# Kernel optimization log

Hardware: AMD Instinct MI355X
Metric: run time of the kernel (lower is better)

## Reference

```python
import jax, jax.numpy as jnp
import numpy as np

D_QUERY = 512
D_AUDIO = 512
D_OUT = 512
B, HW, S = 16, 4096, 1024


def setup_inputs() -> dict:
    key = jax.random.key(0)
    ks = jax.random.split(key, 8)
    sc_q = 1.0 / np.sqrt(D_QUERY)
    sc_a = 1.0 / np.sqrt(D_AUDIO)
    return {
        "x": jax.random.normal(ks[0], (B, HW, D_QUERY), dtype=jnp.float32),
        "audio_embed": jax.random.normal(ks[1], (B, S, D_AUDIO), dtype=jnp.float32),
        "Wq": jax.random.uniform(ks[2], (D_QUERY, D_OUT), jnp.float32, -sc_q, sc_q),
        "bq": jax.random.uniform(ks[3], (D_OUT,), jnp.float32, -sc_q, sc_q),
        "Wk": jax.random.uniform(ks[4], (D_AUDIO, D_OUT), jnp.float32, -sc_a, sc_a),
        "bk": jax.random.uniform(ks[5], (D_OUT,), jnp.float32, -sc_a, sc_a),
        "Wv": jax.random.uniform(ks[6], (D_AUDIO, D_OUT), jnp.float32, -sc_a, sc_a),
        "bv": jax.random.uniform(ks[7], (D_OUT,), jnp.float32, -sc_a, sc_a),
    }


def reference(x, audio_embed, Wq, bq, Wk, bk, Wv, bv):
    # Linear projections (nn.Linear: y = x @ W^T + b; we store W already transposed)
    Q = x @ Wq + bq                      # [B, HW, D_OUT]
    K = audio_embed @ Wk + bk            # [B, S, D_OUT]
    V = audio_embed @ Wv + bv            # [B, S, D_OUT]
    scale = 1.0 / (K.shape[-1] ** 0.5)   # divide by sqrt(d_out), per source
    scores = jnp.einsum("bnd,bsd->bns", Q, K) * scale  # [B, HW, S]
    attn = jax.nn.softmax(scores, axis=-1)
    return jnp.einsum("bns,bsd->bnd", attn, V)         # [B, HW, D_OUT]
```

## Files before the change

kernel.cpp:

```cpp
#include <hip/hip_runtime.h>
#include <hip/hip_bf16.h>

typedef __attribute__((ext_vector_type(8))) short bf16x8;
typedef __attribute__((ext_vector_type(4))) float f32x4;
typedef __attribute__((ext_vector_type(4))) unsigned short ushort4v;

#define AS1 __attribute__((address_space(1)))
#define AS3 __attribute__((address_space(3)))

__device__ __forceinline__ float bf_bits_to_f(short s) {
  unsigned int u = ((unsigned int)(unsigned short)s) << 16;
  union { unsigned int u; float f; } c; c.u = u; return c.f;
}
__device__ __forceinline__ unsigned short f_to_bf_bits(float f) {
  union { float f; unsigned int u; } c; c.f = f;
  unsigned int r = c.u + 0x7FFFu + ((c.u >> 16) & 1u);
  return (unsigned short)(r >> 16);
}

__device__ __forceinline__ int fsw(int row) { return ((row >> 1) & 3) << 4; }

__global__ __launch_bounds__(256) void cvt_bf16_kernel(const float* __restrict__ in,
                                                       unsigned short* __restrict__ out,
                                                       long n) {
  const long nchunks = n >> 2;
  const long stride = (long)gridDim.x * 256;
  for (long c = (long)blockIdx.x * 256 + threadIdx.x; c < nchunks; c += stride) {
    f32x4 v = *(const f32x4*)(in + c * 4);
    ushort4v o;
    o[0] = f_to_bf_bits(v[0]); o[1] = f_to_bf_bits(v[1]);
    o[2] = f_to_bf_bits(v[2]); o[3] = f_to_bf_bits(v[3]);
    *(ushort4v*)(out + c * 4) = o;
  }
}

__global__ __launch_bounds__(256) void transpose_w_kernel(
    const float* __restrict__ W0, const float* __restrict__ W1, const float* __restrict__ W2,
    unsigned short* __restrict__ T0, unsigned short* __restrict__ T1, unsigned short* __restrict__ T2) {
  const float* W = (blockIdx.z == 0) ? W0 : (blockIdx.z == 1) ? W1 : W2;
  unsigned short* T = (blockIdx.z == 0) ? T0 : (blockIdx.z == 1) ? T1 : T2;
  __shared__ float t[32][33];
  const int tx = threadIdx.x & 31, ty = threadIdx.x >> 5;
  const int n0 = blockIdx.x * 32, k0 = blockIdx.y * 32;
#pragma unroll
  for (int j = 0; j < 4; ++j)
    t[ty + 8 * j][tx] = W[(long)(k0 + ty + 8 * j) * 512 + n0 + tx];
  __syncthreads();
#pragma unroll
  for (int j = 0; j < 4; ++j)
    T[(long)(n0 + ty + 8 * j) * 512 + k0 + tx] = f_to_bf_bits(t[tx][ty + 8 * j]);
}

template <bool BIAS, bool TRANSOUT, bool AFP32>
__global__ __launch_bounds__(256) void gemm_kernel(
    const void* __restrict__ Aptr,
    const unsigned short* __restrict__ BT,
    const float* __restrict__ bias,
    unsigned short* __restrict__ Cout,
    const int K, const float scale,
    const long strideA, const long strideBT, const long strideC, const int ldc,
    const int nx, const int ny) {
  __shared__ unsigned short lds[8192];
  const int nwg = gridDim.x;
  const int chunk = nwg >> 3;
  const int bid = blockIdx.x;
  const int swz = (bid & 7) * chunk + (bid >> 3);
  const int bx = swz % nx;
  const int t1 = swz / nx;
  const int by = t1 % ny;
  const int bz = t1 / ny;

  const int tid = threadIdx.x;
  const int lane = tid & 63;
  const int wv = tid >> 6;
  const int wr = wv >> 1, wc = wv & 1;
  const unsigned short* Ab = (const unsigned short*)Aptr + (long)bz * strideA + (long)by * 128 * K;
  const float* Af = (const float*)Aptr + (long)bz * strideA + (long)by * 128 * K;
  const unsigned short* Bb = BT + (long)bz * strideBT + (long)bx * 128 * K;

  f32x4 acc[4][4];
#pragma unroll
  for (int m = 0; m < 4; ++m)
#pragma unroll
    for (int n = 0; n < 4; ++n) acc[m][n] = (f32x4){0.f, 0.f, 0.f, 0.f};

  const int r15 = lane & 15, g = lane >> 4;
  const int kiters = K >> 5;
  const int asw = fsw(r15);

  int arow[2], acs[2];
#pragma unroll
  for (int i = 0; i < 2; ++i) {
    const int c = i * 4 + wv;
    const int boff = c * 1024 + lane * 16;
    arow[i] = boff >> 6;
    acs[i] = (boff & 63) ^ fsw(arow[i]);
  }
  f32x4 pa[2][2];
  if (AFP32) {
#pragma unroll
    for (int i = 0; i < 2; ++i) {
      const float* s = Af + (long)arow[i] * K + (acs[i] >> 1);
      pa[i][0] = *(const f32x4*)s;
      pa[i][1] = *(const f32x4*)(s + 4);
    }
  }

  for (int kt = 0; kt < kiters; ++kt) {
#pragma unroll
    for (int i = 0; i < 2; ++i) {
      const int c = i * 4 + wv;
      const char* srcB = (const char*)Bb + (long)arow[i] * (K * 2) + kt * 64 + acs[i];
      __builtin_amdgcn_global_load_lds(
          (const AS1 void*)srcB, (AS3 void*)(lds + 4096 + c * 512), 16, 0, 0);
      if (!AFP32) {
        const char* srcA = (const char*)Ab + (long)arow[i] * (K * 2) + kt * 64 + acs[i];
        __builtin_amdgcn_global_load_lds(
            (const AS1 void*)srcA, (AS3 void*)(lds + c * 512), 16, 0, 0);
      }
    }
    if (AFP32) {
#pragma unroll
      for (int i = 0; i < 2; ++i) {
        const int c = i * 4 + wv;
        bf16x8 w;
#pragma unroll
        for (int e = 0; e < 4; ++e) {
          w[e] = (short)f_to_bf_bits(pa[i][0][e]);
          w[4 + e] = (short)f_to_bf_bits(pa[i][1][e]);
        }
        *(bf16x8*)&lds[c * 512 + lane * 8] = w;
      }
      if (kt < kiters - 1) {
#pragma unroll
        for (int i = 0; i < 2; ++i) {
          const float* s = Af + (long)arow[i] * K + (kt + 1) * 32 + (acs[i] >> 1);
          pa[i][0] = *(const f32x4*)s;
          pa[i][1] = *(const f32x4*)(s + 4);
        }
      }
    }
    __syncthreads();

    bf16x8 af[4], bf[4];
#pragma unroll
    for (int m = 0; m < 4; ++m)
      af[m] = *(const bf16x8*)((const char*)lds + (wr * 64 + m * 16 + r15) * 64 + (g * 16 ^ asw));
#pragma unroll
    for (int n = 0; n < 4; ++n)
      bf[n] = *(const bf16x8*)((const char*)lds + 8192 +
                               (wc * 64 + n * 16 + r15) * 64 + (g * 16 ^ asw));
#pragma unroll
    for (int m = 0; m < 4; ++m)
#pragma unroll
      for (int n = 0; n < 4; ++n)
        acc[m][n] = __builtin_amdgcn_mfma_f32_16x16x32_bf16(af[m], bf[n], acc[m][n], 0, 0, 0);
    __syncthreads();
  }

  const long crow0 = (long)by * 128 + wr * 64;
  const long ccol0 = (long)bx * 128 + wc * 64;
#pragma unroll
  for (int n = 0; n < 4; ++n) {
    const long col = ccol0 + n * 16 + r15;
    const float bv = BIAS ? bias[col] : 0.f;
#pragma unroll
    for (int m = 0; m < 4; ++m) {
      const f32x4 v = acc[m][n];
#pragma unroll
      for (int j = 0; j < 4; ++j) {
        const long row = crow0 + m * 16 + g * 4 + j;
        const float val = (v[j] + bv) * scale;
        const long idx = TRANSOUT ? (col * (long)ldc + row) : (row * (long)ldc + col);
        (Cout + (long)bz * strideC)[idx] = f_to_bf_bits(val);
      }
    }
  }
}

template <bool EXPSTATS, bool DIVSTATS>
__global__ __launch_bounds__(512, 2) void gemm256_kernel(
    const unsigned short* __restrict__ A,
    const unsigned short* __restrict__ BT,
    void* __restrict__ Cout,
    const int K,
    const long strideA, const long strideBT, const long strideC, const int ldc,
    const int nx, const int ny, float* __restrict__ stats) {
  __shared__ __align__(16) char ring[3][32768];
  __shared__ float ssum[256][4];
  __shared__ float invl[256];

  const int nwg = gridDim.x;
  const int chunk = nwg >> 3;
  const int bid = blockIdx.x;
  const int swz = (bid & 7) * chunk + (bid >> 3);
  const int bx = swz % nx;
  const int t1 = swz / nx;
  const int by = t1 % ny;
  const int bz = t1 / ny;

  const int tid = threadIdx.x;
  const int lane = tid & 63;
  const int w = tid >> 6;
  const int wm = w >> 2, wn = w & 3;
  const int r15 = lane & 15, g = lane >> 4;

  const unsigned short* Ab = A + (long)bz * strideA + (long)by * 256 * K;
  const unsigned short* Bb = BT + (long)bz * strideBT + (long)bx * 256 * K;
  const long rsb = (long)K * 2;

  if (DIVSTATS) {
    if (tid < 256) {
      const f32x4 s = *(const f32x4*)&stats[((long)bz * 4096 + (long)by * 256 + tid) * 4];
      invl[tid] = 1.f / (s[0] + s[1] + s[2] + s[3]);
    }
  }

  const int boff = tid * 16;
  const int srow = boff >> 6;
  const int scol = (boff & 63) ^ fsw(srow);
  const long sOff0 = (long)srow * rsb + scol;
  const long sOff1 = (long)(srow + 128) * rsb + scol;
  const char* Abyt = (const char*)Ab;
  const char* Bbyt = (const char*)Bb;

  auto gl1 = [&](const char* srcBase, long srcOff, char* dstBase, int dstOff) {
    __builtin_amdgcn_global_load_lds((const AS1 void*)(srcBase + srcOff),
                                     (AS3 void*)(dstBase + dstOff), 16, 0, 0);
  };

  f32x4 acc[8][4];
#pragma unroll
  for (int m = 0; m < 8; ++m)
#pragma unroll
    for (int n = 0; n < 4; ++n) acc[m][n] = (f32x4){0.f, 0.f, 0.f, 0.f};

  const int kiters = K >> 5;
  const int asw = fsw(r15);

  gl1(Abyt, sOff0, ring[0], boff);
  gl1(Abyt, sOff1, ring[0], 8192 + boff);
  gl1(Bbyt, sOff0, ring[0], 16384 + boff);
  gl1(Bbyt, sOff1, ring[0], 24576 + boff);
  gl1(Abyt, sOff0 + 64, ring[1], boff);
  gl1(Abyt, sOff1 + 64, ring[1], 8192 + boff);
  gl1(Bbyt, sOff0 + 64, ring[1], 16384 + boff);
  gl1(Bbyt, sOff1 + 64, ring[1], 24576 + boff);

  int cur = 0, sb = 2;
  for (int kt = 0; kt < kiters; ++kt) {
    const char* bA = ring[cur];
    const char* bB = ring[cur] + 16384;
    char* sd = ring[sb];
    const bool st = (kt + 2) < kiters;
    const long kb = (long)(kt + 2) * 64;
    bf16x8 af0[4], af1[4], bf0[2], bf1[2];

    if (kt + 1 < kiters) asm volatile("s_waitcnt vmcnt(4)" ::: "memory");
    else                 asm volatile("s_waitcnt vmcnt(0)" ::: "memory");
    __builtin_amdgcn_s_barrier();
    __builtin_amdgcn_sched_barrier(0);
#pragma unroll
    for (int m = 0; m < 4; ++m)
      af0[m] = *(const bf16x8*)(bA + (wm * 128 + m * 16 + r15) * 64 + ((g * 16) ^ asw));
#pragma unroll
    for (int n = 0; n < 2; ++n)
      bf0[n] = *(const bf16x8*)(bB + (wn * 64 + n * 16 + r15) * 64 + ((g * 16) ^ asw));
    if (st) gl1(Abyt, sOff0 + kb, sd, boff);
    __builtin_amdgcn_s_setprio(1);
#pragma unroll
    for (int m = 0; m < 4; ++m)
#pragma unroll
      for (int n = 0; n < 2; ++n)
        acc[m][n] = __builtin_amdgcn_mfma_f32_16x16x32_bf16(af0[m], bf0[n], acc[m][n], 0, 0, 0);
    __builtin_amdgcn_s_setprio(0);

    __builtin_amdgcn_s_barrier();
    __builtin_amdgcn_sched_barrier(0);
#pragma unroll
    for (int n = 0; n < 2; ++n)
      bf1[n] = *(const bf16x8*)(bB + (wn * 64 + (n + 2) * 16 + r15) * 64 + ((g * 16) ^ asw));
    if (st) gl1(Abyt, sOff1 + kb, sd, 8192 + boff);
    __builtin_amdgcn_s_setprio(1);
#pragma unroll
    for (int m = 0; m < 4; ++m)
#pragma unroll
      for (int n = 0; n < 2; ++n)
        acc[m][2 + n] = __builtin_amdgcn_mfma_f32_16x16x32_bf16(af0[m], bf1[n], acc[m][2 + n], 0, 0, 0);
    __builtin_amdgcn_s_setprio(0);

    __builtin_amdgcn_s_barrier();
    __builtin_amdgcn_sched_barrier(0);
#pragma unroll
    for (int m = 0; m < 4; ++m)
      af1[m] = *(const bf16x8*)(bA + (wm * 128 + (m + 4) * 16 + r15) * 64 + ((g * 16) ^ asw));
    if (st) gl1(Bbyt, sOff0 + kb, sd, 16384 + boff);
    __builtin_amdgcn_s_setprio(1);
#pragma unroll
    for (int m = 0; m < 4; ++m)
#pragma unroll
      for (int n = 0; n < 2; ++n)
        acc[4 + m][2 + n] = __builtin_amdgcn_mfma_f32_16x16x32_bf16(af1[m], bf1[n], acc[4 + m][2 + n], 0, 0, 0);
    __builtin_amdgcn_s_setprio(0);

    __builtin_amdgcn_s_barrier();
    __builtin_amdgcn_sched_barrier(0);
    if (st) gl1(Bbyt, sOff1 + kb, sd, 24576 + boff);
    __builtin_amdgcn_s_setprio(1);
#pragma unroll
    for (int m = 0; m < 4; ++m)
#pragma unroll
      for (int n = 0; n < 2; ++n)
        acc[4 + m][n] = __builtin_amdgcn_mfma_f32_16x16x32_bf16(af1[m], bf0[n], acc[4 + m][n], 0, 0, 0);
    __builtin_amdgcn_s_setprio(0);

    cur = (cur == 2) ? 0 : cur + 1;
    sb = (sb == 2) ? 0 : sb + 1;
  }

  if (EXPSTATS) {
#pragma unroll
    for (int m = 0; m < 8; ++m)
#pragma unroll
      for (int n = 0; n < 4; ++n)
#pragma unroll
        for (int j = 0; j < 4; ++j) acc[m][n][j] = __expf(acc[m][n][j]);
#pragma unroll
    for (int m = 0; m < 8; ++m)
#pragma unroll
      for (int j = 0; j < 4; ++j) {
        float s = acc[m][0][j] + acc[m][1][j] + acc[m][2][j] + acc[m][3][j];
        s += __shfl_xor(s, 1);
        s += __shfl_xor(s, 2);
        s += __shfl_xor(s, 4);
        s += __shfl_xor(s, 8);
        if (r15 == 0) ssum[wm * 128 + m * 16 + g * 4 + j][wn] = s;
      }
    __syncthreads();
    if (tid < 256) {
      const float t = ssum[tid][0] + ssum[tid][1] + ssum[tid][2] + ssum[tid][3];
      stats[((long)bz * 4096 + (long)by * 256 + tid) * 4 + bx] = t;
    }
  }

  const long crow0 = (long)by * 256 + wm * 128;
  const long ccol0 = (long)bx * 256 + wn * 64;
#pragma unroll
  for (int m = 0; m < 8; ++m)
#pragma unroll
    for (int j = 0; j < 4; ++j) {
      const int rl = wm * 128 + m * 16 + g * 4 + j;
      const long row = crow0 + m * 16 + g * 4 + j;
#pragma unroll
      for (int n = 0; n < 4; ++n) {
        const long col = ccol0 + n * 16 + r15;
        if (EXPSTATS) {
          ((unsigned short*)Cout + (long)bz * strideC)[row * (long)ldc + col] =
              f_to_bf_bits(acc[m][n][j]);
        } else {
          const float sc = DIVSTATS ? invl[rl] : 1.f;
          ((float*)Cout + (long)bz * strideC)[row * (long)ldc + col] = acc[m][n][j] * sc;
        }
      }
    }
}

extern "C" void kernel_launch(void* const* d_in, const int* in_sizes, int n_in,
                              void* d_out, int out_size, void* d_ws, size_t ws_size,
                              hipStream_t stream) {
  (void)in_sizes; (void)n_in; (void)out_size; (void)ws_size;
  const float* x     = (const float*)d_in[0];
  const float* audio = (const float*)d_in[1];
  const float* Wq    = (const float*)d_in[2];
  const float* bq    = (const float*)d_in[3];
  const float* Wk    = (const float*)d_in[4];
  const float* bk    = (const float*)d_in[5];
  const float* Wv    = (const float*)d_in[6];
  const float* bv    = (const float*)d_in[7];
  float* out = (float*)d_out;

  char* ws = (char*)d_ws;
  size_t off = 0;
  auto carve = [&](size_t bytes) { char* p = ws + off; off += (bytes + 255) & ~(size_t)255; return p; };
  unsigned short* ab  = (unsigned short*)carve((size_t)16384 * 512 * 2);
  unsigned short* wqt = (unsigned short*)carve((size_t)512 * 512 * 2);
  unsigned short* wkt = (unsigned short*)carve((size_t)512 * 512 * 2);
  unsigned short* wvt = (unsigned short*)carve((size_t)512 * 512 * 2);
  unsigned short* Qb  = (unsigned short*)carve((size_t)65536 * 512 * 2);
  unsigned short* Kb  = (unsigned short*)carve((size_t)16384 * 512 * 2);
  unsigned short* Vt  = (unsigned short*)carve((size_t)16384 * 512 * 2);
  unsigned short* Pb  = (unsigned short*)carve((size_t)65536 * 1024 * 2);
  float*          ls  = (float*)carve((size_t)65536 * 4 * 4);

  cvt_bf16_kernel<<<1024, 256, 0, stream>>>(audio, ab, (long)16384 * 512);
  transpose_w_kernel<<<dim3(16, 16, 3), 256, 0, stream>>>(Wq, Wk, Wv, wqt, wkt, wvt);
  gemm_kernel<true, false, true><<<4 * 512, 256, 0, stream>>>(
      x, wqt, bq, Qb, 512, 0.044194173824159216f, 0, 0, 0, 512, 4, 512);
  gemm_kernel<true, false, false><<<4 * 128, 256, 0, stream>>>(
      ab, wkt, bk, Kb, 512, 1.f, 0, 0, 0, 512, 4, 128);
  gemm_kernel<true, true, false><<<4 * 8 * 16, 256, 0, stream>>>(
      ab, wvt, bv, Vt, 512, 1.f, (long)1024 * 512, 0, (long)512 * 1024, 1024, 4, 8);
  gemm256_kernel<true, false><<<4 * 16 * 16, 512, 0, stream>>>(
      Qb, Kb, Pb, 512,
      (long)4096 * 512, (long)1024 * 512, (long)4096 * 1024, 1024, 4, 16, ls);
  gemm256_kernel<false, true><<<2 * 16 * 16, 512, 0, stream>>>(
      Pb, Vt, out, 1024,
      (long)4096 * 1024, (long)512 * 1024, (long)4096 * 512, 512, 2, 16, ls);
}
```

Baseline: 357.9 us.

## Switch GEMM mainloop to double-buffered 64-wide K tiles with new swizzle

```diff
diff --git a/kernel.cpp b/kernel.cpp
--- a/kernel.cpp
+++ b/kernel.cpp
@@ -186,7 +186,7 @@
     const int K,
     const long strideA, const long strideBT, const long strideC, const int ldc,
     const int nx, const int ny, float* __restrict__ stats) {
-  __shared__ __align__(16) char ring[3][32768];
+  __shared__ __align__(16) char ring[2][65536];
   __shared__ float ssum[256][4];
   __shared__ float invl[256];
 
@@ -204,9 +204,10 @@
   const int w = tid >> 6;
   const int wm = w >> 2, wn = w & 3;
   const int r15 = lane & 15, g = lane >> 4;
-
-  const unsigned short* Ab = A + (long)bz * strideA + (long)by * 256 * K;
-  const unsigned short* Bb = BT + (long)bz * strideBT + (long)bx * 256 * K;
+  const int csw = (r15 & 7) << 4;
+
+  const char* Abyt = (const char*)(A + (long)bz * strideA + (long)by * 256 * K);
+  const char* Bbyt = (const char*)(BT + (long)bz * strideBT + (long)bx * 256 * K);
   const long rsb = (long)K * 2;
 
   if (DIVSTATS) {
@@ -216,18 +217,16 @@
     }
   }
 
-  const int boff = tid * 16;
-  const int srow = boff >> 6;
-  const int scol = (boff & 63) ^ fsw(srow);
-  const long sOff0 = (long)srow * rsb + scol;
-  const long sOff1 = (long)(srow + 128) * rsb + scol;
-  const char* Abyt = (const char*)Ab;
-  const char* Bbyt = (const char*)Bb;
-
-  auto gl1 = [&](const char* srcBase, long srcOff, char* dstBase, int dstOff) {
-    __builtin_amdgcn_global_load_lds((const AS1 void*)(srcBase + srcOff),
-                                     (AS3 void*)(dstBase + dstOff), 16, 0, 0);
-  };
+  long soff[8];
+  int doff[8];
+#pragma unroll
+  for (int j = 0; j < 8; ++j) {
+    const int o = (j & 3) * 8192 + tid * 16;
+    const int row = o >> 7;
+    const int lc = (o >> 4) & 7;
+    soff[j] = (long)row * rsb + ((lc ^ (row & 7)) << 4);
+    doff[j] = ((j < 4) ? 0 : 32768) + o;
+  }
 
   f32x4 acc[8][4];
 #pragma unroll
@@ -235,87 +234,110 @@
 #pragma unroll
     for (int n = 0; n < 4; ++n) acc[m][n] = (f32x4){0.f, 0.f, 0.f, 0.f};
 
-  const int kiters = K >> 5;
-  const int asw = fsw(r15);
-
-  gl1(Abyt, sOff0, ring[0], boff);
-  gl1(Abyt, sOff1, ring[0], 8192 + boff);
-  gl1(Bbyt, sOff0, ring[0], 16384 + boff);
-  gl1(Bbyt, sOff1, ring[0], 24576 + boff);
-  gl1(Abyt, sOff0 + 64, ring[1], boff);
-  gl1(Abyt, sOff1 + 64, ring[1], 8192 + boff);
-  gl1(Bbyt, sOff0 + 64, ring[1], 16384 + boff);
-  gl1(Bbyt, sOff1 + 64, ring[1], 24576 + boff);
-
-  int cur = 0, sb = 2;
+  const int kiters = K >> 6;
+
+#pragma unroll
+  for (int j = 0; j < 8; ++j)
+    __builtin_amdgcn_global_load_lds(
+        (const AS1 void*)(((j < 4) ? Abyt : Bbyt) + soff[j]),
+        (AS3 void*)(ring[0] + doff[j]), 16, 0, 0);
+  asm volatile("s_waitcnt vmcnt(0)" ::: "memory");
+  __builtin_amdgcn_s_barrier();
+  __builtin_amdgcn_sched_barrier(0);
+
   for (int kt = 0; kt < kiters; ++kt) {
-    const char* bA = ring[cur];
-    const char* bB = ring[cur] + 16384;
-    char* sd = ring[sb];
-    const bool st = (kt + 2) < kiters;
-    const long kb = (long)(kt + 2) * 64;
-    bf16x8 af0[4], af1[4], bf0[2], bf1[2];
-
-    if (kt + 1 < kiters) asm volatile("s_waitcnt vmcnt(4)" ::: "memory");
-    else                 asm volatile("s_waitcnt vmcnt(0)" ::: "memory");
+    const char* bA = ring[kt & 1];
+    const char* bB = ring[kt & 1] + 32768;
+    char* bn = ring[(kt + 1) & 1];
+    const bool st = (kt + 1) < kiters;
+    const long kb = (long)(kt + 1) * 128;
+    bf16x8 fa[4], fb[4];
+
+#define PH_SYNC()                                          \
+    __builtin_amdgcn_sched_barrier(0);                     \
+    __builtin_amdgcn_s_barrier();                          \
+    asm volatile("s_waitcnt lgkmcnt(0)" ::: "memory");     \
+    __builtin_amdgcn_sched_barrier(0);
+
+#define PH_END()                                           \
+    __builtin_amdgcn_s_setprio(0);                         \
+    __builtin_amdgcn_sched_barrier(0);                     \
+    __builtin_amdgcn_s_barrier();                          \
+    __builtin_amdgcn_sched_barrier(0);
+
+#pragma unroll
+    for (int m = 0; m < 4; ++m)
+      fa[m] = *(const bf16x8*)(bA + (wm * 128 + m * 16 + r15) * 128 + ((g * 16) ^ csw));
+#pragma unroll
+    for (int n = 0; n < 4; ++n)
+      fb[n] = *(const bf16x8*)(bB + (wn * 64 + n * 16 + r15) * 128 + ((g * 16) ^ csw));
+    if (st) {
+#pragma unroll
+      for (int j = 0; j < 4; ++j)
+        __builtin_amdgcn_global_load_lds((const AS1 void*)(Abyt + soff[j] + kb),
+                                         (AS3 void*)(bn + doff[j]), 16, 0, 0);
+    }
+    PH_SYNC();
+    __builtin_amdgcn_s_setprio(1);
+#pragma unroll
+    for (int m = 0; m < 4; ++m)
+#pragma unroll
+      for (int n = 0; n < 4; ++n)
+        acc[m][n] = __builtin_amdgcn_mfma_f32_16x16x32_bf16(fa[m], fb[n], acc[m][n], 0, 0, 0);
+    PH_END();
+
+#pragma unroll
+    for (int m = 0; m < 4; ++m)
+      fa[m] = *(const bf16x8*)(bA + (wm * 128 + (m + 4) * 16 + r15) * 128 + ((g * 16) ^ csw));
+    if (st) {
+#pragma unroll
+      for (int j = 4; j < 8; ++j)
+        __builtin_amdgcn_global_load_lds((const AS1 void*)(Bbyt + soff[j] + kb),
+                                         (AS3 void*)(bn + doff[j]), 16, 0, 0);
+    }
+    PH_SYNC();
+    __builtin_amdgcn_s_setprio(1);
+#pragma unroll
+    for (int m = 0; m < 4; ++m)
+#pragma unroll
+      for (int n = 0; n < 4; ++n)
+        acc[4 + m][n] = __builtin_amdgcn_mfma_f32_16x16x32_bf16(fa[m], fb[n], acc[4 + m][n], 0, 0, 0);
+    PH_END();
+
+#pragma unroll
+    for (int m = 0; m < 4; ++m)
+      fa[m] = *(const bf16x8*)(bA + (wm * 128 + m * 16 + r15) * 128 + ((64 + g * 16) ^ csw));
+#pragma unroll
+    for (int n = 0; n < 4; ++n)
+      fb[n] = *(const bf16x8*)(bB + (wn * 64 + n * 16 + r15) * 128 + ((64 + g * 16) ^ csw));
+    PH_SYNC();
+    __builtin_amdgcn_s_setprio(1);
+#pragma unroll
+    for (int m = 0; m < 4; ++m)
+#pragma unroll
+      for (int n = 0; n < 4; ++n)
+        acc[m][n] = __builtin_amdgcn_mfma_f32_16x16x32_bf16(fa[m], fb[n], acc[m][n], 0, 0, 0);
+    PH_END();
+
+#pragma unroll
+    for (int m = 0; m < 4; ++m)
+      fa[m] = *(const bf16x8*)(bA + (wm * 128 + (m + 4) * 16 + r15) * 128 + ((64 + g * 16) ^ csw));
+    PH_SYNC();
+    __builtin_amdgcn_s_setprio(1);
+#pragma unroll
+    for (int m = 0; m < 4; ++m)
+#pragma unroll
+      for (int n = 0; n < 4; ++n)
+        acc[4 + m][n] = __builtin_amdgcn_mfma_f32_16x16x32_bf16(fa[m], fb[n], acc[4 + m][n], 0, 0, 0);
+    __builtin_amdgcn_s_setprio(0);
+    __builtin_amdgcn_sched_barrier(0);
+    asm volatile("s_waitcnt vmcnt(0)" ::: "memory");
+    __builtin_amdgcn_sched_barrier(0);
     __builtin_amdgcn_s_barrier();
     __builtin_amdgcn_sched_barrier(0);
-#pragma unroll
-    for (int m = 0; m < 4; ++m)
-      af0[m] = *(const bf16x8*)(bA + (wm * 128 + m * 16 + r15) * 64 + ((g * 16) ^ asw));
-#pragma unroll
-    for (int n = 0; n < 2; ++n)
-      bf0[n] = *(const bf16x8*)(bB + (wn * 64 + n * 16 + r15) * 64 + ((g * 16) ^ asw));
-    if (st) gl1(Abyt, sOff0 + kb, sd, boff);
-    __builtin_amdgcn_s_setprio(1);
-#pragma unroll
-    for (int m = 0; m < 4; ++m)
-#pragma unroll
-      for (int n = 0; n < 2; ++n)
-        acc[m][n] = __builtin_amdgcn_mfma_f32_16x16x32_bf16(af0[m], bf0[n], acc[m][n], 0, 0, 0);
-    __builtin_amdgcn_s_setprio(0);
-
-    __builtin_amdgcn_s_barrier();
-    __builtin_amdgcn_sched_barrier(0);
-#pragma unroll
-    for (int n = 0; n < 2; ++n)
-      bf1[n] = *(const bf16x8*)(bB + (wn * 64 + (n + 2) * 16 + r15) * 64 + ((g * 16) ^ asw));
-    if (st) gl1(Abyt, sOff1 + kb, sd, 8192 + boff);
-    __builtin_amdgcn_s_setprio(1);
-#pragma unroll
-    for (int m = 0; m < 4; ++m)
-#pragma unroll
-      for (int n = 0; n < 2; ++n)
-        acc[m][2 + n] = __builtin_amdgcn_mfma_f32_16x16x32_bf16(af0[m], bf1[n], acc[m][2 + n], 0, 0, 0);
-    __builtin_amdgcn_s_setprio(0);
-
-    __builtin_amdgcn_s_barrier();
-    __builtin_amdgcn_sched_barrier(0);
-#pragma unroll
-    for (int m = 0; m < 4; ++m)
-      af1[m] = *(const bf16x8*)(bA + (wm * 128 + (m + 4) * 16 + r15) * 64 + ((g * 16) ^ asw));
-    if (st) gl1(Bbyt, sOff0 + kb, sd, 16384 + boff);
-    __builtin_amdgcn_s_setprio(1);
-#pragma unroll
-    for (int m = 0; m < 4; ++m)
-#pragma unroll
-      for (int n = 0; n < 2; ++n)
-        acc[4 + m][2 + n] = __builtin_amdgcn_mfma_f32_16x16x32_bf16(af1[m], bf1[n], acc[4 + m][2 + n], 0, 0, 0);
-    __builtin_amdgcn_s_setprio(0);
-
-    __builtin_amdgcn_s_barrier();
-    __builtin_amdgcn_sched_barrier(0);
-    if (st) gl1(Bbyt, sOff1 + kb, sd, 24576 + boff);
-    __builtin_amdgcn_s_setprio(1);
-#pragma unroll
-    for (int m = 0; m < 4; ++m)
-#pragma unroll
-      for (int n = 0; n < 2; ++n)
-        acc[4 + m][n] = __builtin_amdgcn_mfma_f32_16x16x32_bf16(af1[m], bf0[n], acc[4 + m][n], 0, 0, 0);
-    __builtin_amdgcn_s_setprio(0);
-
-    cur = (cur == 2) ? 0 : cur + 1;
-    sb = (sb == 2) ? 0 : sb + 1;
+
+#undef PH_SYNC
+#undef PH_END
   }
 
   if (EXPSTATS) {
```

Result: faster. 338.7 us (-5.4%).
